# Kernel optimization log

Hardware: AMD Instinct MI355X
Metric: run time of the kernel (lower is better)

The kernel has to match this reference:

```python
import jax, jax.numpy as jnp
import numpy as np

N_TOKENS = 131072
E_DIM = 128
CODEBOOK_SIZE = 1024
NUM_Q = 4
BETA = 0.25


def setup_inputs() -> dict:
    key = jax.random.key(0)
    kx, kc = jax.random.split(key)
    x = jax.random.normal(kx, (N_TOKENS, E_DIM), dtype=jnp.float32)
    # nn.Embedding init: uniform(-1/codebook_size, 1/codebook_size)
    codebooks = jax.random.uniform(
        kc, (NUM_Q, CODEBOOK_SIZE, E_DIM), dtype=jnp.float32,
        minval=-1.0 / CODEBOOK_SIZE, maxval=1.0 / CODEBOOK_SIZE)
    return {"x": x, "codebooks": codebooks}


def _quantize_stage(residual, cb, beta):
    # squared euclidean distances (same argmin as torch.cdist): [N, K]
    d = (jnp.sum(residual * residual, axis=1, keepdims=True)
         - 2.0 * residual @ cb.T
         + jnp.sum(cb * cb, axis=1))
    idx = jnp.argmin(d, axis=1)                       # [N]
    q = cb[idx]                                        # gather: [N, E_DIM]
    quantized = residual + jax.lax.stop_gradient(q - residual)  # straight-through
    loss = beta * jnp.mean(jnp.square(residual - jax.lax.stop_gradient(quantized)))
    return quantized, idx, loss


def reference(x, codebooks):
    def step(residual, cb):
        quantized, idx, loss = _quantize_stage(residual, cb, BETA)
        return residual - quantized, (quantized, idx, loss)

    _, (qs, idxs, losses) = jax.lax.scan(step, x, codebooks)
    x_q = jnp.sum(qs, axis=0)          # [N, E_DIM]
    mean_loss = jnp.mean(losses)       # scalar
    all_indices = idxs.T               # [N, NUM_Q], matches torch.stack(dim=-1)
    return x_q, mean_loss, all_indices
```

## Files before the change

### kernel.cpp

```cpp
#include <hip/hip_runtime.h>

#define NT 131072
#define ED 128
#define KCB 1024
#define NQ 4

#define MT 128
#define NBLK (NT / MT)
#define NCH 64
#define NCHUNKS (KCB / NCH)
#define PAIR_CAP 1024
#define MARGIN 1.5e-3f

#define TRL 16384
#define BUFSZ 16640

typedef __attribute__((ext_vector_type(8))) short bf16x8;
typedef __attribute__((ext_vector_type(4))) float f32x4;

#define ASG __attribute__((address_space(1)))
#define ASL __attribute__((address_space(3)))
#define GLOAD_LDS16(g, l) \
    __builtin_amdgcn_global_load_lds((const ASG void*)(g), (ASL void*)(l), 16, 0, 0)

__device__ __forceinline__ unsigned bf16rne(float f) {
    unsigned u = __float_as_uint(f);
    u += 0x7fffu + ((u >> 16) & 1u);
    return u >> 16;
}
__device__ __forceinline__ unsigned packbf(float a, float b) {
    return bf16rne(a) | (bf16rne(b) << 16);
}
__device__ __forceinline__ unsigned fmono(float f) {
    unsigned u = __float_as_uint(f);
    return (u & 0x80000000u) ? ~u : (u | 0x80000000u);
}

__global__ void prep_kernel(const float* __restrict__ cb,
                            float* __restrict__ cnorm,
                            float* __restrict__ loss_slot) {
#pragma clang fp contract(off)
    int c = blockIdx.x * 256 + threadIdx.x;
    if (blockIdx.x == 0 && threadIdx.x == 0) loss_slot[0] = 0.0f;
    const float* row = cb + (size_t)c * ED;
    float r8[8];
#pragma unroll
    for (int m = 0; m < 8; ++m) { float v = row[m]; r8[m] = v * v; }
    for (int i = 8; i < ED; i += 8) {
#pragma unroll
        for (int m = 0; m < 8; ++m) {
            float v = row[i + m];
            float p = v * v;
            r8[m] = r8[m] + p;
        }
    }
    cnorm[c] = ((r8[0] + r8[1]) + (r8[2] + r8[3]))
             + ((r8[4] + r8[5]) + (r8[6] + r8[7]));
}

__global__ void cvt_kernel(const float* __restrict__ cb,
                           unsigned char* __restrict__ cbb) {
#pragma clang fp contract(off)
    int id = blockIdx.x * 256 + threadIdx.x;
    int rg = id >> 4;
    int j  = id & 15;
    const float* src = cb + (size_t)rg * ED + j * 8;
    float4 a = *(const float4*)(src);
    float4 b = *(const float4*)(src + 4);
    uint4 w;
    w.x = packbf(a.x, a.y); w.y = packbf(a.z, a.w);
    w.z = packbf(b.x, b.y); w.w = packbf(b.z, b.w);
    size_t dst = ((size_t)(rg >> 6) << 14)
               + (size_t)((rg & 63) << 8)
               + (size_t)((j ^ (rg & 7)) << 4);
    *(uint4*)(cbb + dst) = w;
}

#define CHAIN4(V, C)                                                     \
    { float d1x = (C).x - (V).x, d1y = (C).y - (V).y,                    \
            d1z = (C).z - (V).z, d1w = (C).w - (V).w;                    \
      float qtx = (V).x + d1x, qty = (V).y + d1y,                        \
            qtz = (V).z + d1z, qtw = (V).w + d1w;                        \
      (V).x = (V).x - qtx; (V).y = (V).y - qty;                          \
      (V).z = (V).z - qtz; (V).w = (V).w - qtw; }

template<int Q>
__device__ __forceinline__ void run_stage(
    const float* __restrict__ x, const float* __restrict__ cb,
    const float* __restrict__ cnorm, const unsigned char* __restrict__ cbb,
    float* __restrict__ d_out,
    unsigned char* U, unsigned long long* selMin, float* Ss,
    unsigned short* selSh, unsigned* pairList, int* pairCnt,
    int tid, int lane, int wid, int l15, int quad, int t0, unsigned xorT) {
#pragma clang fp contract(off)
    const float* cbq = cb + (size_t)Q * KCB * ED;
    const unsigned char* cbbq = cbb + ((size_t)Q << 18);
    const float* cnq = cnorm + Q * KCB;

    if (tid < MT) selMin[tid] = ~0ull;
    if (tid == 0) *pairCnt = 0;
    __syncthreads();

    if (tid < MT) {
        int t = tid;
        const float* xr = x + (size_t)(t0 + t) * ED;
        const float* hp[Q > 0 ? Q : 1];
#pragma unroll
        for (int p2 = 0; p2 < Q; ++p2)
            hp[p2] = cb + ((size_t)p2 * KCB + (int)selSh[t * NQ + p2]) * ED;
        unsigned char* Aw = U + t * 256;
        unsigned xw = (unsigned)((t & 7) << 4);
        float r8[8];
#pragma unroll
        for (int m = 0; m < 8; ++m) r8[m] = 0.f;
#pragma unroll 4
        for (int i = 0; i < 32; ++i) {
            float4 v = *(const float4*)(xr + (i << 2));
#pragma unroll
            for (int p2 = 0; p2 < Q; ++p2) {
                float4 c = *(const float4*)(hp[p2] + (i << 2));
                CHAIN4(v, c)
            }
            uint2 w2;
            w2.x = packbf(v.x, v.y); w2.y = packbf(v.z, v.w);
            *(uint2*)(Aw + (((((unsigned)(i >> 1)) << 4) ^ xw)
                            | ((unsigned)(i & 1) << 3))) = w2;
            int base = (i & 1) << 2;
            float px = v.x * v.x, py = v.y * v.y,
                  pz = v.z * v.z, pw = v.w * v.w;
            r8[base + 0] = r8[base + 0] + px;
            r8[base + 1] = r8[base + 1] + py;
            r8[base + 2] = r8[base + 2] + pz;
            r8[base + 3] = r8[base + 3] + pw;
        }
        Ss[t] = ((r8[0] + r8[1]) + (r8[2] + r8[3]))
              + ((r8[4] + r8[5]) + (r8[6] + r8[7]));
    }
    __syncthreads();

    bf16x8 bfrag[2][4];
#pragma unroll
    for (int tt = 0; tt < 2; ++tt)
#pragma unroll
        for (int ks = 0; ks < 4; ++ks) {
            int tok = wid * 32 + tt * 16 + l15;
            bfrag[tt][ks] = *(const bf16x8*)(U + tok * 256 +
                (((unsigned)(ks * 64 + quad * 16)) ^ xorT));
        }
    __syncthreads();

    {
        const unsigned char* src = cbbq + (wid << 12) + (lane << 4);
        unsigned char* dst = U + (wid << 12) + (lane << 4);
        GLOAD_LDS16(src,        dst);
        GLOAD_LDS16(src + 1024, dst + 1024);
        GLOAD_LDS16(src + 2048, dst + 2048);
        GLOAD_LDS16(src + 3072, dst + 3072);
        if (lane < 16)
            GLOAD_LDS16((const unsigned char*)cnq + (lane << 4),
                        U + TRL + (lane << 4));
    }

    float rmin[2] = {1e30f, 1e30f};
    for (int cc = 0; cc < NCHUNKS; ++cc) {
        const int cur = cc & 1;

        __builtin_amdgcn_s_barrier();
        __builtin_amdgcn_sched_barrier(0);

        if (cc + 1 < NCHUNKS) {
            const unsigned char* src = cbbq + ((size_t)(cc + 1) << 14)
                                     + (wid << 12) + (lane << 4);
            unsigned char* dst = U + (cur ^ 1) * BUFSZ
                               + (wid << 12) + (lane << 4);
            GLOAD_LDS16(src,        dst);
            GLOAD_LDS16(src + 1024, dst + 1024);
            GLOAD_LDS16(src + 2048, dst + 2048);
            GLOAD_LDS16(src + 3072, dst + 3072);
            if (lane < 16)
                GLOAD_LDS16((const unsigned char*)(cnq + (cc + 1) * NCH)
                                + (lane << 4),
                            U + (cur ^ 1) * BUFSZ + TRL + (lane << 4));
            __builtin_amdgcn_sched_barrier(0);
            asm volatile("s_waitcnt vmcnt(5)" ::: "memory");
        } else {
            __builtin_amdgcn_sched_barrier(0);
            asm volatile("s_waitcnt vmcnt(0)" ::: "memory");
        }
        __builtin_amdgcn_s_barrier();
        __builtin_amdgcn_sched_barrier(0);

        f32x4 acc[4][2];
#pragma unroll
        for (int ct = 0; ct < 4; ++ct)
#pragma unroll
            for (int tt = 0; tt < 2; ++tt)
                acc[ct][tt] = (f32x4){0.f, 0.f, 0.f, 0.f};
        const unsigned char* Ub = U + cur * BUFSZ;
#pragma unroll
        for (int ks = 0; ks < 4; ++ks) {
            bf16x8 afr[4];
#pragma unroll
            for (int ct = 0; ct < 4; ++ct)
                afr[ct] = *(const bf16x8*)(Ub + (ct * 16 + l15) * 256 +
                    (((unsigned)(ks * 64 + quad * 16)) ^ xorT));
#pragma unroll
            for (int ct = 0; ct < 4; ++ct)
#pragma unroll
                for (int tt = 0; tt < 2; ++tt)
                    acc[ct][tt] = __builtin_amdgcn_mfma_f32_16x16x32_bf16(
                        afr[ct], bfrag[tt][ks], acc[ct][tt], 0, 0, 0);
        }

        const float* cnL = (const float*)(Ub + TRL);
        float tmin[2] = {1e30f, 1e30f};
#pragma unroll
        for (int ct = 0; ct < 4; ++ct) {
            f32x4 cn4 = *(const f32x4*)(cnL + ct * 16 + quad * 4);
#pragma unroll
            for (int tt = 0; tt < 2; ++tt)
#pragma unroll
                for (int r2 = 0; r2 < 4; ++r2) {
                    float m2 = acc[ct][tt][r2];
                    float e = cn4[r2] - (m2 + m2);
                    acc[ct][tt][r2] = e;
                    tmin[tt] = fminf(tmin[tt], e);
                }
        }
#pragma unroll
        for (int tt = 0; tt < 2; ++tt) {
            float v = tmin[tt];
            v = fminf(v, __shfl_xor(v, 16, 64));
            v = fminf(v, __shfl_xor(v, 32, 64));
            rmin[tt] = fminf(rmin[tt], v);
        }

#pragma unroll
        for (int tt = 0; tt < 2; ++tt) {
            int token = wid * 32 + tt * 16 + l15;
            float th = rmin[tt] + MARGIN;
#pragma unroll
            for (int ct = 0; ct < 4; ++ct)
#pragma unroll
                for (int r2 = 0; r2 < 4; ++r2) {
                    float e = acc[ct][tt][r2];
                    if (e <= th) {
                        int code = cc * NCH + ct * 16 + quad * 4 + r2;
                        int pos = atomicAdd(pairCnt, 1);
                        if (pos < PAIR_CAP)
                            pairList[pos] =
                                ((unsigned)token << 10) | (unsigned)code;
                    }
                }
        }
    }
    __syncthreads();

    {
        int npair = *pairCnt < PAIR_CAP ? *pairCnt : PAIR_CAP;
        for (int p = tid; p < npair; p += 256) {
            unsigned pk = pairList[p];
            int t = (pk >> 10) & 127, code = pk & 1023;
            const float* xr = x + (size_t)(t0 + t) * ED;
            const float* cr = cbq + (size_t)code * ED;
            const float* hp[Q > 0 ? Q : 1];
#pragma unroll
            for (int p2 = 0; p2 < Q; ++p2)
                hp[p2] = cb + ((size_t)p2 * KCB + (int)selSh[t * NQ + p2]) * ED;
            float M = 0.f;
#pragma unroll 4
            for (int k = 0; k < ED; k += 4) {
                float4 v = *(const float4*)(xr + k);
#pragma unroll
                for (int p2 = 0; p2 < Q; ++p2) {
                    float4 c = *(const float4*)(hp[p2] + k);
                    CHAIN4(v, c)
                }
                float4 cv = *(const float4*)(cr + k);
                M = fmaf(v.x, cv.x, M); M = fmaf(v.y, cv.y, M);
                M = fmaf(v.z, cv.z, M); M = fmaf(v.w, cv.w, M);
            }
            float t1 = Ss[t] - (M + M);
            float dd = t1 + cnorm[Q * KCB + code];
            unsigned long long key =
                ((unsigned long long)fmono(dd) << 10) | (unsigned)code;
            unsigned long long old = selMin[t];
            while (key < old) {
                unsigned long long assumed = old;
                old = atomicCAS(&selMin[t], assumed, key);
                if (old == assumed) break;
            }
        }
    }
    __syncthreads();

    if (tid < MT) {
        int code = (int)(selMin[tid] & 1023ull);
        selSh[tid * NQ + Q] = (unsigned short)code;
        d_out[(size_t)NT * ED + 1 + (size_t)(t0 + tid) * NQ + Q] = (float)code;
    }
    __syncthreads();
}

__global__ __launch_bounds__(256, 3) void rvq_mfma(const float* __restrict__ x,
                                                   const float* __restrict__ cb,
                                                   const float* __restrict__ cnorm,
                                                   const unsigned char* __restrict__ cbb,
                                                   float* __restrict__ d_out) {
#pragma clang fp contract(off)
    __shared__ __align__(16) unsigned char U[2 * BUFSZ];
    __shared__ unsigned long long selMin[MT];
    __shared__ float    Ss[MT];
    __shared__ unsigned short selSh[MT * NQ];
    __shared__ unsigned pairList[PAIR_CAP];
    __shared__ int      pairCnt;
    __shared__ double   lossW[4];

    const int tid  = threadIdx.x;
    const int lane = tid & 63;
    const int wid  = tid >> 6;
    const int l15  = lane & 15;
    const int quad = lane >> 4;
    const int t0   = blockIdx.x * MT;
    const unsigned xorT = (unsigned)((l15 & 7) << 4);

    run_stage<0>(x, cb, cnorm, cbb, d_out, U, selMin, Ss, selSh,
                 pairList, &pairCnt, tid, lane, wid, l15, quad, t0, xorT);
    run_stage<1>(x, cb, cnorm, cbb, d_out, U, selMin, Ss, selSh,
                 pairList, &pairCnt, tid, lane, wid, l15, quad, t0, xorT);
    run_stage<2>(x, cb, cnorm, cbb, d_out, U, selMin, Ss, selSh,
                 pairList, &pairCnt, tid, lane, wid, l15, quad, t0, xorT);
    run_stage<3>(x, cb, cnorm, cbb, d_out, U, selMin, Ss, selSh,
                 pairList, &pairCnt, tid, lane, wid, l15, quad, t0, xorT);

    double lossTot = 0.0;
    if (tid < MT) {
        int t = tid;
        const float* xr = x + (size_t)(t0 + t) * ED;
        const float* hp[4];
#pragma unroll
        for (int p2 = 0; p2 < NQ; ++p2)
            hp[p2] = cb + ((size_t)p2 * KCB + (int)selSh[t * NQ + p2]) * ED;
        double lo = 0.0;
#pragma unroll 4
        for (int k = 0; k < ED; k += 4) {
            float4 v = *(const float4*)(xr + k);
            float4 o = v;
#pragma unroll
            for (int p2 = 0; p2 < NQ; ++p2) {
                float4 c = *(const float4*)(hp[p2] + k);
                CHAIN4(v, c)
                lo += (double)v.x * v.x + (double)v.y * v.y
                    + (double)v.z * v.z + (double)v.w * v.w;
            }
            float4 xq;
            xq.x = o.x - v.x; xq.y = o.y - v.y;
            xq.z = o.z - v.z; xq.w = o.w - v.w;
            *(float4*)(d_out + (size_t)(t0 + t) * ED + k) = xq;
        }
        lossTot = lo;
    }

    double l = lossTot;
#pragma unroll
    for (int off = 32; off > 0; off >>= 1) l += __shfl_down(l, off, 64);
    if ((tid & 63) == 0) lossW[tid >> 6] = l;
    __syncthreads();
    if (tid == 0) {
        double s = lossW[0] + lossW[1] + lossW[2] + lossW[3];
        atomicAdd(d_out + (size_t)NT * ED, (float)(s * (0.25 / (4.0 * (double)NT * ED))));
    }
}

extern "C" void kernel_launch(void* const* d_in, const int* in_sizes, int n_in,
                              void* d_out, int out_size, void* d_ws, size_t ws_size,
                              hipStream_t stream) {
    const float* x  = (const float*)d_in[0];
    const float* cb = (const float*)d_in[1];
    float* out   = (float*)d_out;
    float* cnorm = (float*)d_ws;
    unsigned char* cbb = (unsigned char*)d_ws + 16384;

    prep_kernel<<<16, 256, 0, stream>>>(cb, cnorm, out + (size_t)NT * ED);
    cvt_kernel<<<256, 256, 0, stream>>>(cb, cbb);
    rvq_mfma<<<NBLK, 256, 0, stream>>>(x, cb, cnorm, cbb, out);
}
```

Before: 990.6 us.

## Split fused RVQ kernel into per-stage residual and selection kernels

Splits the single fused four-stage kernel into a residual/bf16-pack kernel and a selection kernel per stage, followed by a separate epilogue kernel. Residuals, norms and selected indices now pass through workspace global memory instead of LDS. The aim is to run the residual computation with every thread rather than half the block, and to let each kernel tune occupancy on its own. In exchange it adds nine launches and about 32 MB of global traffic per stage, plus unswizzled B-fragment loads from global memory. A fallback keeps the old monolithic kernel when the workspace is too small.

```diff
diff --git a/kernel.cpp b/kernel.cpp
--- a/kernel.cpp
+++ b/kernel.cpp
@@ -84,58 +84,79 @@
       (V).x = (V).x - qtx; (V).y = (V).y - qty;                          \
       (V).z = (V).z - qtz; (V).w = (V).w - qtw; }
 
+
 template<int Q>
-__device__ __forceinline__ void run_stage(
+__global__ void s_kernel(const float* __restrict__ x,
+                         const float* __restrict__ cb,
+                         const unsigned short* __restrict__ selG,
+                         unsigned char* __restrict__ As,
+                         float* __restrict__ SsG) {
+#pragma clang fp contract(off)
+    int t = blockIdx.x * 256 + threadIdx.x;
+    const float* xr = x + (size_t)t * ED;
+    const float* hp[Q > 0 ? Q : 1];
+#pragma unroll
+    for (int p2 = 0; p2 < Q; ++p2)
+        hp[p2] = cb + ((size_t)p2 * KCB + (int)selG[t * NQ + p2]) * ED;
+    unsigned char* Aw = As + (size_t)t * 256;
+    float r8[8];
+#pragma unroll
+    for (int m = 0; m < 8; ++m) r8[m] = 0.f;
+    unsigned w0 = 0, w1 = 0;
+#pragma unroll 4
+    for (int i = 0; i < 32; ++i) {
+        float4 v = *(const float4*)(xr + (i << 2));
+#pragma unroll
+        for (int p2 = 0; p2 < Q; ++p2) {
+            float4 c = *(const float4*)(hp[p2] + (i << 2));
+            CHAIN4(v, c)
+        }
+        if ((i & 1) == 0) {
+            w0 = packbf(v.x, v.y); w1 = packbf(v.z, v.w);
+        } else {
+            uint4 w;
+            w.x = w0; w.y = w1;
+            w.z = packbf(v.x, v.y); w.w = packbf(v.z, v.w);
+            *(uint4*)(Aw + ((i >> 1) << 4)) = w;
+        }
+        int base = (i & 1) << 2;
+        float px = v.x * v.x, py = v.y * v.y,
+              pz = v.z * v.z, pw = v.w * v.w;
+        r8[base + 0] = r8[base + 0] + px;
+        r8[base + 1] = r8[base + 1] + py;
+        r8[base + 2] = r8[base + 2] + pz;
+        r8[base + 3] = r8[base + 3] + pw;
+    }
+    SsG[t] = ((r8[0] + r8[1]) + (r8[2] + r8[3]))
+           + ((r8[4] + r8[5]) + (r8[6] + r8[7]));
+}
+
+template<int Q>
+__global__ __launch_bounds__(256, 3) void select_kernel(
     const float* __restrict__ x, const float* __restrict__ cb,
     const float* __restrict__ cnorm, const unsigned char* __restrict__ cbb,
-    float* __restrict__ d_out,
-    unsigned char* U, unsigned long long* selMin, float* Ss,
-    unsigned short* selSh, unsigned* pairList, int* pairCnt,
-    int tid, int lane, int wid, int l15, int quad, int t0, unsigned xorT) {
+    const unsigned char* __restrict__ As, const float* __restrict__ SsG,
+    unsigned short* __restrict__ selG, float* __restrict__ d_out) {
 #pragma clang fp contract(off)
+    __shared__ __align__(16) unsigned char U[2 * BUFSZ];
+    __shared__ unsigned long long selMin[MT];
+    __shared__ unsigned pairList[PAIR_CAP];
+    __shared__ int      pairCnt;
+
+    const int tid  = threadIdx.x;
+    const int lane = tid & 63;
+    const int wid  = tid >> 6;
+    const int l15  = lane & 15;
+    const int quad = lane >> 4;
+    const int t0   = blockIdx.x * MT;
+    const unsigned xorT = (unsigned)((l15 & 7) << 4);
+
     const float* cbq = cb + (size_t)Q * KCB * ED;
     const unsigned char* cbbq = cbb + ((size_t)Q << 18);
     const float* cnq = cnorm + Q * KCB;
 
     if (tid < MT) selMin[tid] = ~0ull;
-    if (tid == 0) *pairCnt = 0;
-    __syncthreads();
-
-    if (tid < MT) {
-        int t = tid;
-        const float* xr = x + (size_t)(t0 + t) * ED;
-        const float* hp[Q > 0 ? Q : 1];
-#pragma unroll
-        for (int p2 = 0; p2 < Q; ++p2)
-            hp[p2] = cb + ((size_t)p2 * KCB + (int)selSh[t * NQ + p2]) * ED;
-        unsigned char* Aw = U + t * 256;
-        unsigned xw = (unsigned)((t & 7) << 4);
-        float r8[8];
-#pragma unroll
-        for (int m = 0; m < 8; ++m) r8[m] = 0.f;
-#pragma unroll 4
-        for (int i = 0; i < 32; ++i) {
-            float4 v = *(const float4*)(xr + (i << 2));
-#pragma unroll
-            for (int p2 = 0; p2 < Q; ++p2) {
-                float4 c = *(const float4*)(hp[p2] + (i << 2));
-                CHAIN4(v, c)
-            }
-            uint2 w2;
-            w2.x = packbf(v.x, v.y); w2.y = packbf(v.z, v.w);
-            *(uint2*)(Aw + (((((unsigned)(i >> 1)) << 4) ^ xw)
-                            | ((unsigned)(i & 1) << 3))) = w2;
-            int base = (i & 1) << 2;
-            float px = v.x * v.x, py = v.y * v.y,
-                  pz = v.z * v.z, pw = v.w * v.w;
-            r8[base + 0] = r8[base + 0] + px;
-            r8[base + 1] = r8[base + 1] + py;
-            r8[base + 2] = r8[base + 2] + pz;
-            r8[base + 3] = r8[base + 3] + pw;
-        }
-        Ss[t] = ((r8[0] + r8[1]) + (r8[2] + r8[3]))
-              + ((r8[4] + r8[5]) + (r8[6] + r8[7]));
-    }
+    if (tid == 0) pairCnt = 0;
     __syncthreads();
 
     bf16x8 bfrag[2][4];
@@ -143,11 +164,10 @@
     for (int tt = 0; tt < 2; ++tt)
 #pragma unroll
         for (int ks = 0; ks < 4; ++ks) {
-            int tok = wid * 32 + tt * 16 + l15;
-            bfrag[tt][ks] = *(const bf16x8*)(U + tok * 256 +
-                (((unsigned)(ks * 64 + quad * 16)) ^ xorT));
-        }
-    __syncthreads();
+            int tok = t0 + wid * 32 + tt * 16 + l15;
+            bfrag[tt][ks] = *(const bf16x8*)(As + (size_t)tok * 256
+                                             + ks * 64 + quad * 16);
+        }
 
     {
         const unsigned char* src = cbbq + (wid << 12) + (lane << 4);
@@ -246,6 +266,262 @@
                     float e = acc[ct][tt][r2];
                     if (e <= th) {
                         int code = cc * NCH + ct * 16 + quad * 4 + r2;
+                        int pos = atomicAdd(&pairCnt, 1);
+                        if (pos < PAIR_CAP)
+                            pairList[pos] =
+                                ((unsigned)token << 10) | (unsigned)code;
+                    }
+                }
+        }
+    }
+    __syncthreads();
+
+    {
+        int npair = pairCnt < PAIR_CAP ? pairCnt : PAIR_CAP;
+        for (int p = tid; p < npair; p += 256) {
+            unsigned pk = pairList[p];
+            int t = (pk >> 10) & 127, code = pk & 1023;
+            const float* xr = x + (size_t)(t0 + t) * ED;
+            const float* cr = cbq + (size_t)code * ED;
+            const float* hp[Q > 0 ? Q : 1];
+#pragma unroll
+            for (int p2 = 0; p2 < Q; ++p2)
+                hp[p2] = cb + ((size_t)p2 * KCB
+                               + (int)selG[(size_t)(t0 + t) * NQ + p2]) * ED;
+            float M = 0.f;
+#pragma unroll 4
+            for (int k = 0; k < ED; k += 4) {
+                float4 v = *(const float4*)(xr + k);
+#pragma unroll
+                for (int p2 = 0; p2 < Q; ++p2) {
+                    float4 c = *(const float4*)(hp[p2] + k);
+                    CHAIN4(v, c)
+                }
+                float4 cv = *(const float4*)(cr + k);
+                M = fmaf(v.x, cv.x, M); M = fmaf(v.y, cv.y, M);
+                M = fmaf(v.z, cv.z, M); M = fmaf(v.w, cv.w, M);
+            }
+            float t1 = SsG[t0 + t] - (M + M);
+            float dd = t1 + cnorm[Q * KCB + code];
+            unsigned long long key =
+                ((unsigned long long)fmono(dd) << 10) | (unsigned)code;
+            unsigned long long old = selMin[t];
+            while (key < old) {
+                unsigned long long assumed = old;
+                old = atomicCAS(&selMin[t], assumed, key);
+                if (old == assumed) break;
+            }
+        }
+    }
+    __syncthreads();
+
+    if (tid < MT) {
+        int code = (int)(selMin[tid] & 1023ull);
+        selG[(size_t)(t0 + tid) * NQ + Q] = (unsigned short)code;
+        d_out[(size_t)NT * ED + 1 + (size_t)(t0 + tid) * NQ + Q] = (float)code;
+    }
+}
+
+__global__ void epilogue_kernel(const float* __restrict__ x,
+                                const float* __restrict__ cb,
+                                const unsigned short* __restrict__ selG,
+                                float* __restrict__ d_out) {
+#pragma clang fp contract(off)
+    __shared__ double lossW[4];
+    int tid = threadIdx.x;
+    int t = blockIdx.x * 256 + tid;
+    const float* xr = x + (size_t)t * ED;
+    const float* hp[4];
+#pragma unroll
+    for (int p2 = 0; p2 < NQ; ++p2)
+        hp[p2] = cb + ((size_t)p2 * KCB + (int)selG[t * NQ + p2]) * ED;
+    double lo = 0.0;
+#pragma unroll 4
+    for (int k = 0; k < ED; k += 4) {
+        float4 v = *(const float4*)(xr + k);
+        float4 o = v;
+#pragma unroll
+        for (int p2 = 0; p2 < NQ; ++p2) {
+            float4 c = *(const float4*)(hp[p2] + k);
+            CHAIN4(v, c)
+            lo += (double)v.x * v.x + (double)v.y * v.y
+                + (double)v.z * v.z + (double)v.w * v.w;
+        }
+        float4 xq;
+        xq.x = o.x - v.x; xq.y = o.y - v.y;
+        xq.z = o.z - v.z; xq.w = o.w - v.w;
+        *(float4*)(d_out + (size_t)t * ED + k) = xq;
+    }
+#pragma unroll
+    for (int off = 32; off > 0; off >>= 1) lo += __shfl_down(lo, off, 64);
+    if ((tid & 63) == 0) lossW[tid >> 6] = lo;
+    __syncthreads();
+    if (tid == 0) {
+        double s = lossW[0] + lossW[1] + lossW[2] + lossW[3];
+        atomicAdd(d_out + (size_t)NT * ED,
+                  (float)(s * (0.25 / (4.0 * (double)NT * ED))));
+    }
+}
+
+template<int Q>
+__device__ __forceinline__ void run_stage_mono(
+    const float* __restrict__ x, const float* __restrict__ cb,
+    const float* __restrict__ cnorm, const unsigned char* __restrict__ cbb,
+    float* __restrict__ d_out,
+    unsigned char* U, unsigned long long* selMin, float* Ss,
+    unsigned short* selSh, unsigned* pairList, int* pairCnt,
+    int tid, int lane, int wid, int l15, int quad, int t0, unsigned xorT) {
+#pragma clang fp contract(off)
+    const float* cbq = cb + (size_t)Q * KCB * ED;
+    const unsigned char* cbbq = cbb + ((size_t)Q << 18);
+    const float* cnq = cnorm + Q * KCB;
+
+    if (tid < MT) selMin[tid] = ~0ull;
+    if (tid == 0) *pairCnt = 0;
+    __syncthreads();
+
+    if (tid < MT) {
+        int t = tid;
+        const float* xr = x + (size_t)(t0 + t) * ED;
+        const float* hp[Q > 0 ? Q : 1];
+#pragma unroll
+        for (int p2 = 0; p2 < Q; ++p2)
+            hp[p2] = cb + ((size_t)p2 * KCB + (int)selSh[t * NQ + p2]) * ED;
+        unsigned char* Aw = U + t * 256;
+        unsigned xw = (unsigned)((t & 7) << 4);
+        float r8[8];
+#pragma unroll
+        for (int m = 0; m < 8; ++m) r8[m] = 0.f;
+#pragma unroll 4
+        for (int i = 0; i < 32; ++i) {
+            float4 v = *(const float4*)(xr + (i << 2));
+#pragma unroll
+            for (int p2 = 0; p2 < Q; ++p2) {
+                float4 c = *(const float4*)(hp[p2] + (i << 2));
+                CHAIN4(v, c)
+            }
+            uint2 w2;
+            w2.x = packbf(v.x, v.y); w2.y = packbf(v.z, v.w);
+            *(uint2*)(Aw + (((((unsigned)(i >> 1)) << 4) ^ xw)
+                            | ((unsigned)(i & 1) << 3))) = w2;
+            int base = (i & 1) << 2;
+            float px = v.x * v.x, py = v.y * v.y,
+                  pz = v.z * v.z, pw = v.w * v.w;
+            r8[base + 0] = r8[base + 0] + px;
+            r8[base + 1] = r8[base + 1] + py;
+            r8[base + 2] = r8[base + 2] + pz;
+            r8[base + 3] = r8[base + 3] + pw;
+        }
+        Ss[t] = ((r8[0] + r8[1]) + (r8[2] + r8[3]))
+              + ((r8[4] + r8[5]) + (r8[6] + r8[7]));
+    }
+    __syncthreads();
+
+    bf16x8 bfrag[2][4];
+#pragma unroll
+    for (int tt = 0; tt < 2; ++tt)
+#pragma unroll
+        for (int ks = 0; ks < 4; ++ks) {
+            int tok = wid * 32 + tt * 16 + l15;
+            bfrag[tt][ks] = *(const bf16x8*)(U + tok * 256 +
+                (((unsigned)(ks * 64 + quad * 16)) ^ xorT));
+        }
+    __syncthreads();
+
+    {
+        const unsigned char* src = cbbq + (wid << 12) + (lane << 4);
+        unsigned char* dst = U + (wid << 12) + (lane << 4);
+        GLOAD_LDS16(src,        dst);
+        GLOAD_LDS16(src + 1024, dst + 1024);
+        GLOAD_LDS16(src + 2048, dst + 2048);
+        GLOAD_LDS16(src + 3072, dst + 3072);
+        if (lane < 16)
+            GLOAD_LDS16((const unsigned char*)cnq + (lane << 4),
+                        U + TRL + (lane << 4));
+    }
+
+    float rmin[2] = {1e30f, 1e30f};
+    for (int cc = 0; cc < NCHUNKS; ++cc) {
+        const int cur = cc & 1;
+        __builtin_amdgcn_s_barrier();
+        __builtin_amdgcn_sched_barrier(0);
+        if (cc + 1 < NCHUNKS) {
+            const unsigned char* src = cbbq + ((size_t)(cc + 1) << 14)
+                                     + (wid << 12) + (lane << 4);
+            unsigned char* dst = U + (cur ^ 1) * BUFSZ
+                               + (wid << 12) + (lane << 4);
+            GLOAD_LDS16(src,        dst);
+            GLOAD_LDS16(src + 1024, dst + 1024);
+            GLOAD_LDS16(src + 2048, dst + 2048);
+            GLOAD_LDS16(src + 3072, dst + 3072);
+            if (lane < 16)
+                GLOAD_LDS16((const unsigned char*)(cnq + (cc + 1) * NCH)
+                                + (lane << 4),
+                            U + (cur ^ 1) * BUFSZ + TRL + (lane << 4));
+            __builtin_amdgcn_sched_barrier(0);
+            asm volatile("s_waitcnt vmcnt(5)" ::: "memory");
+        } else {
+            __builtin_amdgcn_sched_barrier(0);
+            asm volatile("s_waitcnt vmcnt(0)" ::: "memory");
+        }
+        __builtin_amdgcn_s_barrier();
+        __builtin_amdgcn_sched_barrier(0);
+
+        f32x4 acc[4][2];
+#pragma unroll
+        for (int ct = 0; ct < 4; ++ct)
+#pragma unroll
+            for (int tt = 0; tt < 2; ++tt)
+                acc[ct][tt] = (f32x4){0.f, 0.f, 0.f, 0.f};
+        const unsigned char* Ub = U + cur * BUFSZ;
+#pragma unroll
+        for (int ks = 0; ks < 4; ++ks) {
+            bf16x8 afr[4];
+#pragma unroll
+            for (int ct = 0; ct < 4; ++ct)
+                afr[ct] = *(const bf16x8*)(Ub + (ct * 16 + l15) * 256 +
+                    (((unsigned)(ks * 64 + quad * 16)) ^ xorT));
+#pragma unroll
+            for (int ct = 0; ct < 4; ++ct)
+#pragma unroll
+                for (int tt = 0; tt < 2; ++tt)
+                    acc[ct][tt] = __builtin_amdgcn_mfma_f32_16x16x32_bf16(
+                        afr[ct], bfrag[tt][ks], acc[ct][tt], 0, 0, 0);
+        }
+
+        const float* cnL = (const float*)(Ub + TRL);
+        float tmin[2] = {1e30f, 1e30f};
+#pragma unroll
+        for (int ct = 0; ct < 4; ++ct) {
+            f32x4 cn4 = *(const f32x4*)(cnL + ct * 16 + quad * 4);
+#pragma unroll
+            for (int tt = 0; tt < 2; ++tt)
+#pragma unroll
+                for (int r2 = 0; r2 < 4; ++r2) {
+                    float m2 = acc[ct][tt][r2];
+                    float e = cn4[r2] - (m2 + m2);
+                    acc[ct][tt][r2] = e;
+                    tmin[tt] = fminf(tmin[tt], e);
+                }
+        }
+#pragma unroll
+        for (int tt = 0; tt < 2; ++tt) {
+            float v = tmin[tt];
+            v = fminf(v, __shfl_xor(v, 16, 64));
+            v = fminf(v, __shfl_xor(v, 32, 64));
+            rmin[tt] = fminf(rmin[tt], v);
+        }
+#pragma unroll
+        for (int tt = 0; tt < 2; ++tt) {
+            int token = wid * 32 + tt * 16 + l15;
+            float th = rmin[tt] + MARGIN;
+#pragma unroll
+            for (int ct = 0; ct < 4; ++ct)
+#pragma unroll
+                for (int r2 = 0; r2 < 4; ++r2) {
+                    float e = acc[ct][tt][r2];
+                    if (e <= th) {
+                        int code = cc * NCH + ct * 16 + quad * 4 + r2;
                         int pos = atomicAdd(pairCnt, 1);
                         if (pos < PAIR_CAP)
                             pairList[pos] =
@@ -302,7 +578,7 @@
     __syncthreads();
 }
 
-__global__ __launch_bounds__(256, 3) void rvq_mfma(const float* __restrict__ x,
+__global__ __launch_bounds__(256, 3) void rvq_mono(const float* __restrict__ x,
                                                    const float* __restrict__ cb,
                                                    const float* __restrict__ cnorm,
                                                    const unsigned char* __restrict__ cbb,
@@ -324,14 +600,14 @@
     const int t0   = blockIdx.x * MT;
     const unsigned xorT = (unsigned)((l15 & 7) << 4);
 
-    run_stage<0>(x, cb, cnorm, cbb, d_out, U, selMin, Ss, selSh,
-                 pairList, &pairCnt, tid, lane, wid, l15, quad, t0, xorT);
-    run_stage<1>(x, cb, cnorm, cbb, d_out, U, selMin, Ss, selSh,
-                 pairList, &pairCnt, tid, lane, wid, l15, quad, t0, xorT);
-    run_stage<2>(x, cb, cnorm, cbb, d_out, U, selMin, Ss, selSh,
-                 pairList, &pairCnt, tid, lane, wid, l15, quad, t0, xorT);
-    run_stage<3>(x, cb, cnorm, cbb, d_out, U, selMin, Ss, selSh,
-                 pairList, &pairCnt, tid, lane, wid, l15, quad, t0, xorT);
+    run_stage_mono<0>(x, cb, cnorm, cbb, d_out, U, selMin, Ss, selSh,
+                      pairList, &pairCnt, tid, lane, wid, l15, quad, t0, xorT);
+    run_stage_mono<1>(x, cb, cnorm, cbb, d_out, U, selMin, Ss, selSh,
+                      pairList, &pairCnt, tid, lane, wid, l15, quad, t0, xorT);
+    run_stage_mono<2>(x, cb, cnorm, cbb, d_out, U, selMin, Ss, selSh,
+                      pairList, &pairCnt, tid, lane, wid, l15, quad, t0, xorT);
+    run_stage_mono<3>(x, cb, cnorm, cbb, d_out, U, selMin, Ss, selSh,
+                      pairList, &pairCnt, tid, lane, wid, l15, quad, t0, xorT);
 
     double lossTot = 0.0;
     if (tid < MT) {
@@ -360,7 +636,6 @@
         }
         lossTot = lo;
     }
-
     double l = lossTot;
 #pragma unroll
     for (int off = 32; off > 0; off >>= 1) l += __shfl_down(l, off, 64);
@@ -368,7 +643,8 @@
     __syncthreads();
     if (tid == 0) {
         double s = lossW[0] + lossW[1] + lossW[2] + lossW[3];
-        atomicAdd(d_out + (size_t)NT * ED, (float)(s * (0.25 / (4.0 * (double)NT * ED))));
+        atomicAdd(d_out + (size_t)NT * ED,
+                  (float)(s * (0.25 / (4.0 * (double)NT * ED))));
     }
 }
 
@@ -378,10 +654,29 @@
     const float* x  = (const float*)d_in[0];
     const float* cb = (const float*)d_in[1];
     float* out   = (float*)d_out;
-    float* cnorm = (float*)d_ws;
-    unsigned char* cbb = (unsigned char*)d_ws + 16384;
+    unsigned char* ws = (unsigned char*)d_ws;
+
+    float* cnorm = (float*)ws;
+    unsigned char* cbb = ws + 16384;
+    unsigned short* selG = (unsigned short*)(ws + 16384 + (1u << 20));
+    float* SsG = (float*)(ws + 16384 + (2u << 20));
+    unsigned char* As = ws + 16384 + (2u << 20) + (1u << 19);
+    const size_t need = 16384 + (2ull << 20) + (1ull << 19) + (32ull << 20);
 
     prep_kernel<<<16, 256, 0, stream>>>(cb, cnorm, out + (size_t)NT * ED);
     cvt_kernel<<<256, 256, 0, stream>>>(cb, cbb);
-    rvq_mfma<<<NBLK, 256, 0, stream>>>(x, cb, cnorm, cbb, out);
-}
+
+    if (ws_size >= need) {
+        s_kernel<0><<<NT / 256, 256, 0, stream>>>(x, cb, selG, As, SsG);
+        select_kernel<0><<<NBLK, 256, 0, stream>>>(x, cb, cnorm, cbb, As, SsG, selG, out);
+        s_kernel<1><<<NT / 256, 256, 0, stream>>>(x, cb, selG, As, SsG);
+        select_kernel<1><<<NBLK, 256, 0, stream>>>(x, cb, cnorm, cbb, As, SsG, selG, out);
+        s_kernel<2><<<NT / 256, 256, 0, stream>>>(x, cb, selG, As, SsG);
+        select_kernel<2><<<NBLK, 256, 0, stream>>>(x, cb, cnorm, cbb, As, SsG, selG, out);
+        s_kernel<3><<<NT / 256, 256, 0, stream>>>(x, cb, selG, As, SsG);
+        select_kernel<3><<<NBLK, 256, 0, stream>>>(x, cb, cnorm, cbb, As, SsG, selG, out);
+        epilogue_kernel<<<NT / 256, 256, 0, stream>>>(x, cb, selG, out);
+    } else {
+        rvq_mono<<<NBLK, 256, 0, stream>>>(x, cb, cnorm, cbb, out);
+    }
+}
```

Measured after the change: 1.179 ms. 19.1% more time.
